# Optimization experiments

Measured on AMD Instinct MI355X. Metric: run time of the kernel, lower is better.

The kernel has to match this reference:

```python
import jax, jax.numpy as jnp
import numpy as np

K_SIZE = 5  # kernel_size


def _patches(f, k):
    # f: (b, c, h, w) -> (b, c, k*k, h, w), matching torch.nn.Unfold ordering
    # (patch positions row-major (kh, kw) per channel), padding = k//2, stride 1.
    p = k // 2
    b, c, h, w = f.shape
    fp = jnp.pad(f, ((0, 0), (0, 0), (p, p), (p, p)))
    slices = [fp[:, :, i:i + h, j:j + w] for i in range(k) for j in range(k)]
    return jnp.stack(slices, axis=2)


def _conv1x1(w, b, f):
    # w: (out, in), b: (out,), f: (b, in, h, w)
    return jnp.einsum('oc,bchw->bohw', w, f) + b[None, :, None, None]


def setup_inputs() -> dict:
    key = jax.random.key(0)
    ks = jax.random.split(key, 8)
    B, XC, YC, FT, H, W = 4, 64, 64, 64, 128, 128
    x = jax.random.normal(ks[0], (B, XC, H, W), dtype=jnp.float32)
    y = jax.random.normal(ks[1], (B, YC, H, W), dtype=jnp.float32)
    sx = 1.0 / np.sqrt(XC)
    sy = 1.0 / np.sqrt(YC)
    sf = 1.0 / np.sqrt(FT)
    wx = jax.random.uniform(ks[2], (FT, XC), jnp.float32, -sx, sx)
    bx = jax.random.uniform(ks[3], (FT,), jnp.float32, -sx, sx)
    wy = jax.random.uniform(ks[4], (FT, YC), jnp.float32, -sy, sy)
    by = jax.random.uniform(ks[5], (FT,), jnp.float32, -sy, sy)
    wo = jax.random.uniform(ks[6], (XC, FT), jnp.float32, -sf, sf)
    bo = jax.random.uniform(ks[7], (XC,), jnp.float32, -sf, sf)
    return {"x": x, "y": y, "wx": wx, "bx": bx, "wy": wy, "by": by, "wo": wo, "bo": bo}


def reference(x, y, wx, bx, wy, by, wo, bo):
    k = K_SIZE
    q = _conv1x1(wy, by, y)            # (b, feat, h, w): Q (the q axis of size 1 is squeezed)
    Kp = _patches(q, k)                # (b, feat, k^2, h, w): unfold(conv_y(y))
    v = _conv1x1(wx, bx, x)            # (b, feat, h, w)
    Vp = _patches(v, k)                # (b, feat, k^2, h, w): unfold(conv_x(x))
    A = jnp.einsum('bckhw,bchw->bkhw', Kp, q)   # scores over k^2 neighbors
    A = jax.nn.softmax(A, axis=1)               # softmax over dim=1 (k^2)
    out = jnp.einsum('bkhw,bckhw->bchw', A, Vp)  # aggregate values
    out = _conv1x1(wo, bo, out)
    return out + x
```

## Files before the change

kernel.cpp:

```cpp
#include <hip/hip_runtime.h>

#define HH   128
#define WW   128
#define HW   (HH * WW)
#define CC   64
#define TILE 8
#define HALO 12
#define NHP  (HALO * HALO)

typedef unsigned int uint32;
typedef _Float16 h2   __attribute__((ext_vector_type(2)));
typedef __fp16   h2b  __attribute__((ext_vector_type(2)));
typedef _Float16 h8   __attribute__((ext_vector_type(8)));
typedef float    f32x4 __attribute__((ext_vector_type(4)));

__device__ __forceinline__ uint32 pkrtz(float a, float b) {
    h2b r = __builtin_amdgcn_cvt_pkrtz(a, b);
    return __builtin_bit_cast(uint32, r);
}
__device__ __forceinline__ float dot2(uint32 a, uint32 b, float c) {
#if __has_builtin(__builtin_amdgcn_fdot2)
    return __builtin_amdgcn_fdot2(__builtin_bit_cast(h2b, a),
                                  __builtin_bit_cast(h2b, b), c, false);
#else
    h2 x = __builtin_bit_cast(h2, a), y = __builtin_bit_cast(h2, b);
    return c + (float)x.x * (float)y.x + (float)x.y * (float)y.y;
#endif
}
__device__ __forceinline__ f32x4 mfma16(uint4 a, uint4 b, f32x4 c) {
    return __builtin_amdgcn_mfma_f32_16x16x32_f16(
        __builtin_bit_cast(h8, a), __builtin_bit_cast(h8, b), c, 0, 0, 0);
}
__device__ __forceinline__ uint4 pack_w8(const float* __restrict__ w) {
    const float4 lo = *(const float4*)w;
    const float4 hi = *(const float4*)(w + 4);
    uint4 r;
    r.x = pkrtz(lo.x, lo.y); r.y = pkrtz(lo.z, lo.w);
    r.z = pkrtz(hi.x, hi.y); r.w = pkrtz(hi.z, hi.w);
    return r;
}

__global__ __launch_bounds__(256, 4)
void fused_attn(const float* __restrict__ x, const float* __restrict__ y,
                const float* __restrict__ wx, const float* __restrict__ bx,
                const float* __restrict__ wy, const float* __restrict__ by,
                const float* __restrict__ wo, const float* __restrict__ bo,
                float* __restrict__ out)
{
    __shared__ uint32 Ah[NHP * 32];
    __shared__ uint32 Bh[NHP * 32];

    const int lin  = blockIdx.x;
    const int xcd  = lin & 7;
    const int rr   = lin >> 3;
    const int b    = xcd >> 1;
    const int half = xcd & 1;
    const int ty0  = (((rr >> 4) + half * 8)) * TILE;
    const int tx0  = (rr & 15) * TILE;

    const int t = threadIdx.x;

    for (int i = t; i < NHP * 8; i += 256) {
        const int c   = i / NHP;
        const int pix = i - c * NHP;
        const int hy  = pix / HALO, hx = pix - hy * HALO;
        int gy = ty0 + hy - 2, gx = tx0 + hx - 2;
        const bool ok = ((unsigned)gy < HH) & ((unsigned)gx < WW);
        if (!ok) { gy = 0; gx = 0; }
        const size_t base = (size_t)b * CC * HW + (size_t)(c * 8) * HW
                          + (size_t)gy * WW + gx;
        float yv[8], xv[8];
        #pragma unroll
        for (int j = 0; j < 8; ++j) {
            yv[j] = y[base + (size_t)j * HW];
            xv[j] = x[base + (size_t)j * HW];
        }
        uint4 yq, xq;
        yq.x = pkrtz(yv[0], yv[1]); yq.y = pkrtz(yv[2], yv[3]);
        yq.z = pkrtz(yv[4], yv[5]); yq.w = pkrtz(yv[6], yv[7]);
        xq.x = pkrtz(xv[0], xv[1]); xq.y = pkrtz(xv[2], xv[3]);
        xq.z = pkrtz(xv[4], xv[5]); xq.w = pkrtz(xv[6], xv[7]);
        const int w0 = (c ^ (pix & 7)) * 4;
        *(uint4*)&Ah[pix * 32 + w0] = yq;
        *(uint4*)&Bh[pix * 32 + w0] = xq;
    }
    __syncthreads();

    const int wv = t >> 6;
    const int ln = t & 63;
    const int lm = ln & 15;
    const int qd = ln >> 4;

    f32x4 accq[9], accv[9];
    uint2 xres[4];
    {
        const uint4 aq0 = pack_w8(wy + (wv * 16 + lm) * CC + qd * 8);
        const uint4 aq1 = pack_w8(wy + (wv * 16 + lm) * CC + qd * 8 + 32);
        const uint4 av0 = pack_w8(wx + (wv * 16 + lm) * CC + qd * 8);
        const uint4 av1 = pack_w8(wx + (wv * 16 + lm) * CC + qd * 8 + 32);
        #pragma unroll
        for (int nt = 0; nt < 9; ++nt) {
            const int px = nt * 16 + lm, sw = px & 7;
            const uint4 b0 = *(const uint4*)&Ah[px * 32 + ((qd    ) ^ sw) * 4];
            const uint4 b1 = *(const uint4*)&Ah[px * 32 + ((qd + 4) ^ sw) * 4];
            f32x4 a = {0.f, 0.f, 0.f, 0.f};
            a = mfma16(aq0, b0, a); a = mfma16(aq1, b1, a); accq[nt] = a;
            const uint4 c0 = *(const uint4*)&Bh[px * 32 + ((qd    ) ^ sw) * 4];
            const uint4 c1 = *(const uint4*)&Bh[px * 32 + ((qd + 4) ^ sw) * 4];
            f32x4 v = {0.f, 0.f, 0.f, 0.f};
            v = mfma16(av0, c0, v); v = mfma16(av1, c1, v); accv[nt] = v;
        }
        #pragma unroll
        for (int nt = 0; nt < 4; ++nt) {
            const int px = nt * 16 + lm;
            const int hpix = ((px >> 3) + 2) * HALO + (px & 7) + 2;
            const int chunk = wv * 2 + (qd >> 1);
            xres[nt] = *(const uint2*)
                &Bh[hpix * 32 + (chunk ^ (hpix & 7)) * 4 + (qd & 1) * 2];
        }
    }
    __syncthreads();

    {
        const float4 bq = *(const float4*)(by + wv * 16 + qd * 4);
        const float4 bv = *(const float4*)(bx + wv * 16 + qd * 4);
        const int chunk = wv * 2 + (qd >> 1);
        #pragma unroll
        for (int nt = 0; nt < 9; ++nt) {
            const int px = nt * 16 + lm;
            const int hy = px / HALO, hx = px - hy * HALO;
            const int gy = ty0 + hy - 2, gx = tx0 + hx - 2;
            uint2 wq = {0u, 0u}, wvv = {0u, 0u};
            if (((unsigned)gy < HH) & ((unsigned)gx < WW)) {
                wq.x  = pkrtz(accq[nt].x + bq.x, accq[nt].y + bq.y);
                wq.y  = pkrtz(accq[nt].z + bq.z, accq[nt].w + bq.w);
                wvv.x = pkrtz(accv[nt].x + bv.x, accv[nt].y + bv.y);
                wvv.y = pkrtz(accv[nt].z + bv.z, accv[nt].w + bv.w);
            }
            const int off = px * 32 + (chunk ^ (px & 7)) * 4 + (qd & 1) * 2;
            *(uint2*)&Ah[off] = wq;
            *(uint2*)&Bh[off] = wvv;
        }
    }
    __syncthreads();

    const int p    = t >> 2, sub = t & 3;
    const int py   = p >> 3, px8 = p & 7;
    const int crow = (py + 2) * HALO + (px8 + 2);

    uint32 qc[8];
    {
        const int c0 = ((2 * sub) ^ (crow & 7)) * 4;
        const int c1 = ((2 * sub + 1) ^ (crow & 7)) * 4;
        *(uint4*)&qc[0] = *(const uint4*)&Ah[crow * 32 + c0];
        *(uint4*)&qc[4] = *(const uint4*)&Ah[crow * 32 + c1];
    }

    float sc[25];
    #pragma unroll
    for (int dy = 0; dy < 5; ++dy)
        #pragma unroll
        for (int dx = 0; dx < 5; ++dx) {
            const int nrow = (py + dy) * HALO + (px8 + dx);
            const int c0 = ((2 * sub) ^ (nrow & 7)) * 4;
            const int c1 = ((2 * sub + 1) ^ (nrow & 7)) * 4;
            const uint4 r0 = *(const uint4*)&Ah[nrow * 32 + c0];
            const uint4 r1 = *(const uint4*)&Ah[nrow * 32 + c1];
            float s = 0.f;
            s = dot2(qc[0], r0.x, s); s = dot2(qc[1], r0.y, s);
            s = dot2(qc[2], r0.z, s); s = dot2(qc[3], r0.w, s);
            s = dot2(qc[4], r1.x, s); s = dot2(qc[5], r1.y, s);
            s = dot2(qc[6], r1.z, s); s = dot2(qc[7], r1.w, s);
            s += __shfl_xor(s, 1);
            s += __shfl_xor(s, 2);
            sc[dy * 5 + dx] = s;
        }

    float mx = sc[0];
    #pragma unroll
    for (int k = 1; k < 25; ++k) mx = fmaxf(mx, sc[k]);
    float sum = 0.f;
    #pragma unroll
    for (int k = 0; k < 25; ++k) { sc[k] = __expf(sc[k] - mx); sum += sc[k]; }
    const float inv = 1.f / sum;

    h2 ag[8];
    #pragma unroll
    for (int k = 0; k < 8; ++k) ag[k] = (h2)(_Float16)0;
    #pragma unroll
    for (int dy = 0; dy < 5; ++dy)
        #pragma unroll
        for (int dx = 0; dx < 5; ++dx) {
            const int nrow = (py + dy) * HALO + (px8 + dx);
            const int c0 = ((2 * sub) ^ (nrow & 7)) * 4;
            const int c1 = ((2 * sub + 1) ^ (nrow & 7)) * 4;
            const uint4 r0 = *(const uint4*)&Bh[nrow * 32 + c0];
            const uint4 r1 = *(const uint4*)&Bh[nrow * 32 + c1];
            const _Float16 af = (_Float16)(sc[dy * 5 + dx] * inv);
            const h2 a2 = {af, af};
            ag[0] += a2 * __builtin_bit_cast(h2, r0.x);
            ag[1] += a2 * __builtin_bit_cast(h2, r0.y);
            ag[2] += a2 * __builtin_bit_cast(h2, r0.z);
            ag[3] += a2 * __builtin_bit_cast(h2, r0.w);
            ag[4] += a2 * __builtin_bit_cast(h2, r1.x);
            ag[5] += a2 * __builtin_bit_cast(h2, r1.y);
            ag[6] += a2 * __builtin_bit_cast(h2, r1.z);
            ag[7] += a2 * __builtin_bit_cast(h2, r1.w);
        }

    __syncthreads();
    {
        const int c0 = ((2 * sub) ^ (p & 7)) * 4;
        const int c1 = ((2 * sub + 1) ^ (p & 7)) * 4;
        uint4 w0, w1;
        w0.x = __builtin_bit_cast(uint32, ag[0]); w0.y = __builtin_bit_cast(uint32, ag[1]);
        w0.z = __builtin_bit_cast(uint32, ag[2]); w0.w = __builtin_bit_cast(uint32, ag[3]);
        w1.x = __builtin_bit_cast(uint32, ag[4]); w1.y = __builtin_bit_cast(uint32, ag[5]);
        w1.z = __builtin_bit_cast(uint32, ag[6]); w1.w = __builtin_bit_cast(uint32, ag[7]);
        *(uint4*)&Ah[p * 32 + c0] = w0;
        *(uint4*)&Ah[p * 32 + c1] = w1;
    }
    __syncthreads();

    {
        const uint4 a0 = pack_w8(wo + (wv * 16 + lm) * CC + qd * 8);
        const uint4 a1 = pack_w8(wo + (wv * 16 + lm) * CC + qd * 8 + 32);
        const float4 bq = *(const float4*)(bo + wv * 16 + qd * 4);
        #pragma unroll
        for (int nt = 0; nt < 4; ++nt) {
            const int px = nt * 16 + lm, sw = px & 7;
            const uint4 b0 = *(const uint4*)&Ah[px * 32 + ((qd    ) ^ sw) * 4];
            const uint4 b1 = *(const uint4*)&Ah[px * 32 + ((qd + 4) ^ sw) * 4];
            f32x4 a = {0.f, 0.f, 0.f, 0.f};
            a = mfma16(a0, b0, a);
            a = mfma16(a1, b1, a);
            const int gh = ty0 + (px >> 3), gw = tx0 + (px & 7);
            const h2 xp0 = __builtin_bit_cast(h2, xres[nt].x);
            const h2 xp1 = __builtin_bit_cast(h2, xres[nt].y);
            const float rv[4] = {(float)xp0.x, (float)xp0.y,
                                 (float)xp1.x, (float)xp1.y};
            const float av4[4] = {a.x + bq.x, a.y + bq.y, a.z + bq.z, a.w + bq.w};
            #pragma unroll
            for (int r = 0; r < 4; ++r) {
                const int oc = wv * 16 + qd * 4 + r;
                const size_t ad = (size_t)(b * CC + oc) * HW + (size_t)gh * WW + gw;
                out[ad] = av4[r] + rv[r];
            }
        }
    }
}

extern "C" void kernel_launch(void* const* d_in, const int* in_sizes, int n_in,
                              void* d_out, int out_size, void* d_ws, size_t ws_size,
                              hipStream_t stream) {
    const float* x  = (const float*)d_in[0];
    const float* y  = (const float*)d_in[1];
    const float* wx = (const float*)d_in[2];
    const float* bx = (const float*)d_in[3];
    const float* wy = (const float*)d_in[4];
    const float* by = (const float*)d_in[5];
    const float* wo = (const float*)d_in[6];
    const float* bo = (const float*)d_in[7];
    float* out = (float*)d_out;
    (void)d_ws; (void)ws_size;

    fused_attn<<<dim3(1024), 256, 0, stream>>>(x, y, wx, bx, wy, by, wo, bo, out);
}
```

Measured before the change: 115.9 us.

## Split Q and V projections into separate phases to overlap V with scoring

Separates the Q and V 1x1-conv MFMA phases so that Q is finished and written to shared memory first. The V projection then runs before a barrier placed after the softmax, which lets the score and softmax work interleave with V writes across waves and cuts the live accumulator registers from 18 to 9 vectors. The softmax normalization moves from each of the 25 weights to a single half-precision multiply on the 8 aggregated values. This adds an extra barrier and changes fp16 rounding, since unnormalized exponentials are accumulated in fp16 before scaling.

```diff
diff --git a/kernel.cpp b/kernel.cpp
--- a/kernel.cpp
+++ b/kernel.cpp
@@ -90,14 +90,12 @@
     const int ln = t & 63;
     const int lm = ln & 15;
     const int qd = ln >> 4;
-
-    f32x4 accq[9], accv[9];
-    uint2 xres[4];
+    const int chunk = wv * 2 + (qd >> 1);
+
     {
         const uint4 aq0 = pack_w8(wy + (wv * 16 + lm) * CC + qd * 8);
         const uint4 aq1 = pack_w8(wy + (wv * 16 + lm) * CC + qd * 8 + 32);
-        const uint4 av0 = pack_w8(wx + (wv * 16 + lm) * CC + qd * 8);
-        const uint4 av1 = pack_w8(wx + (wv * 16 + lm) * CC + qd * 8 + 32);
+        f32x4 accq[9];
         #pragma unroll
         for (int nt = 0; nt < 9; ++nt) {
             const int px = nt * 16 + lm, sw = px & 7;
@@ -105,6 +103,31 @@
             const uint4 b1 = *(const uint4*)&Ah[px * 32 + ((qd + 4) ^ sw) * 4];
             f32x4 a = {0.f, 0.f, 0.f, 0.f};
             a = mfma16(aq0, b0, a); a = mfma16(aq1, b1, a); accq[nt] = a;
+        }
+        __syncthreads();
+        const float4 bq = *(const float4*)(by + wv * 16 + qd * 4);
+        #pragma unroll
+        for (int nt = 0; nt < 9; ++nt) {
+            const int px = nt * 16 + lm;
+            const int hy = px / HALO, hx = px - hy * HALO;
+            const int gy = ty0 + hy - 2, gx = tx0 + hx - 2;
+            uint2 wq = {0u, 0u};
+            if (((unsigned)gy < HH) & ((unsigned)gx < WW)) {
+                wq.x = pkrtz(accq[nt].x + bq.x, accq[nt].y + bq.y);
+                wq.y = pkrtz(accq[nt].z + bq.z, accq[nt].w + bq.w);
+            }
+            *(uint2*)&Ah[px * 32 + (chunk ^ (px & 7)) * 4 + (qd & 1) * 2] = wq;
+        }
+    }
+
+    uint2 xres[4];
+    {
+        const uint4 av0 = pack_w8(wx + (wv * 16 + lm) * CC + qd * 8);
+        const uint4 av1 = pack_w8(wx + (wv * 16 + lm) * CC + qd * 8 + 32);
+        f32x4 accv[9];
+        #pragma unroll
+        for (int nt = 0; nt < 9; ++nt) {
+            const int px = nt * 16 + lm, sw = px & 7;
             const uint4 c0 = *(const uint4*)&Bh[px * 32 + ((qd    ) ^ sw) * 4];
             const uint4 c1 = *(const uint4*)&Bh[px * 32 + ((qd + 4) ^ sw) * 4];
             f32x4 v = {0.f, 0.f, 0.f, 0.f};
@@ -114,35 +137,24 @@
         for (int nt = 0; nt < 4; ++nt) {
             const int px = nt * 16 + lm;
             const int hpix = ((px >> 3) + 2) * HALO + (px & 7) + 2;
-            const int chunk = wv * 2 + (qd >> 1);
             xres[nt] = *(const uint2*)
                 &Bh[hpix * 32 + (chunk ^ (hpix & 7)) * 4 + (qd & 1) * 2];
         }
-    }
-    __syncthreads();
-
-    {
-        const float4 bq = *(const float4*)(by + wv * 16 + qd * 4);
+        __syncthreads();
         const float4 bv = *(const float4*)(bx + wv * 16 + qd * 4);
-        const int chunk = wv * 2 + (qd >> 1);
         #pragma unroll
         for (int nt = 0; nt < 9; ++nt) {
             const int px = nt * 16 + lm;
             const int hy = px / HALO, hx = px - hy * HALO;
             const int gy = ty0 + hy - 2, gx = tx0 + hx - 2;
-            uint2 wq = {0u, 0u}, wvv = {0u, 0u};
+            uint2 wvv = {0u, 0u};
             if (((unsigned)gy < HH) & ((unsigned)gx < WW)) {
-                wq.x  = pkrtz(accq[nt].x + bq.x, accq[nt].y + bq.y);
-                wq.y  = pkrtz(accq[nt].z + bq.z, accq[nt].w + bq.w);
                 wvv.x = pkrtz(accv[nt].x + bv.x, accv[nt].y + bv.y);
                 wvv.y = pkrtz(accv[nt].z + bv.z, accv[nt].w + bv.w);
             }
-            const int off = px * 32 + (chunk ^ (px & 7)) * 4 + (qd & 1) * 2;
-            *(uint2*)&Ah[off] = wq;
-            *(uint2*)&Bh[off] = wvv;
-        }
-    }
-    __syncthreads();
+            *(uint2*)&Bh[px * 32 + (chunk ^ (px & 7)) * 4 + (qd & 1) * 2] = wvv;
+        }
+    }
 
     const int p    = t >> 2, sub = t & 3;
     const int py   = p >> 3, px8 = p & 7;
@@ -184,6 +196,8 @@
     for (int k = 0; k < 25; ++k) { sc[k] = __expf(sc[k] - mx); sum += sc[k]; }
     const float inv = 1.f / sum;
 
+    __syncthreads();
+
     h2 ag[8];
     #pragma unroll
     for (int k = 0; k < 8; ++k) ag[k] = (h2)(_Float16)0;
@@ -196,7 +210,7 @@
             const int c1 = ((2 * sub + 1) ^ (nrow & 7)) * 4;
             const uint4 r0 = *(const uint4*)&Bh[nrow * 32 + c0];
             const uint4 r1 = *(const uint4*)&Bh[nrow * 32 + c1];
-            const _Float16 af = (_Float16)(sc[dy * 5 + dx] * inv);
+            const _Float16 af = (_Float16)sc[dy * 5 + dx];
             const h2 a2 = {af, af};
             ag[0] += a2 * __builtin_bit_cast(h2, r0.x);
             ag[1] += a2 * __builtin_bit_cast(h2, r0.y);
@@ -210,6 +224,10 @@
 
     __syncthreads();
     {
+        const _Float16 ih = (_Float16)inv;
+        const h2 i2 = {ih, ih};
+        #pragma unroll
+        for (int k = 0; k < 8; ++k) ag[k] *= i2;
         const int c0 = ((2 * sub) ^ (p & 7)) * 4;
         const int c1 = ((2 * sub + 1) ^ (p & 7)) * 4;
         uint4 w0, w1;
```

After: 119.5 us. +3.1%, slower.

## Transpose output MFMA for float4 stores, hoist weight loads, defer softmax normalization

Applied to the files above, without the earlier changes.

Swaps the MFMA operands in the output projection so that each lane holds four consecutive pixels of one output channel. This lets the result be written with a single float4 store instead of four scattered scalar stores, and the residual x values are gathered from LDS to match that layout. It also hoists all weight and bias loads to the kernel start so they overlap the halo load. The 1/sum softmax scale moves from each of the 25 neighbor weights to a single multiply of the fp16 accumulators, which changes rounding slightly.

```diff
diff --git a/kernel.cpp b/kernel.cpp
--- a/kernel.cpp
+++ b/kernel.cpp
@@ -58,7 +58,22 @@
     const int ty0  = (((rr >> 4) + half * 8)) * TILE;
     const int tx0  = (rr & 15) * TILE;
 
-    const int t = threadIdx.x;
+    const int t  = threadIdx.x;
+    const int wv = t >> 6;
+    const int ln = t & 63;
+    const int lm = ln & 15;
+    const int qd = ln >> 4;
+    const int chunk = wv * 2 + (qd >> 1);
+
+    const uint4 aq0 = pack_w8(wy + (wv * 16 + lm) * CC + qd * 8);
+    const uint4 aq1 = pack_w8(wy + (wv * 16 + lm) * CC + qd * 8 + 32);
+    const uint4 av0 = pack_w8(wx + (wv * 16 + lm) * CC + qd * 8);
+    const uint4 av1 = pack_w8(wx + (wv * 16 + lm) * CC + qd * 8 + 32);
+    const uint4 ao0 = pack_w8(wo + (wv * 16 + lm) * CC + qd * 8);
+    const uint4 ao1 = pack_w8(wo + (wv * 16 + lm) * CC + qd * 8 + 32);
+    const float4 bq = *(const float4*)(by + wv * 16 + qd * 4);
+    const float4 bv = *(const float4*)(bx + wv * 16 + qd * 4);
+    const float  boL = bo[wv * 16 + lm];
 
     for (int i = t; i < NHP * 8; i += 256) {
         const int c   = i / NHP;
@@ -86,18 +101,9 @@
     }
     __syncthreads();
 
-    const int wv = t >> 6;
-    const int ln = t & 63;
-    const int lm = ln & 15;
-    const int qd = ln >> 4;
-
     f32x4 accq[9], accv[9];
-    uint2 xres[4];
-    {
-        const uint4 aq0 = pack_w8(wy + (wv * 16 + lm) * CC + qd * 8);
-        const uint4 aq1 = pack_w8(wy + (wv * 16 + lm) * CC + qd * 8 + 32);
-        const uint4 av0 = pack_w8(wx + (wv * 16 + lm) * CC + qd * 8);
-        const uint4 av1 = pack_w8(wx + (wv * 16 + lm) * CC + qd * 8 + 32);
+    float xres[16];
+    {
         #pragma unroll
         for (int nt = 0; nt < 9; ++nt) {
             const int px = nt * 16 + lm, sw = px & 7;
@@ -110,21 +116,22 @@
             f32x4 v = {0.f, 0.f, 0.f, 0.f};
             v = mfma16(av0, c0, v); v = mfma16(av1, c1, v); accv[nt] = v;
         }
-        #pragma unroll
-        for (int nt = 0; nt < 4; ++nt) {
-            const int px = nt * 16 + lm;
-            const int hpix = ((px >> 3) + 2) * HALO + (px & 7) + 2;
-            const int chunk = wv * 2 + (qd >> 1);
-            xres[nt] = *(const uint2*)
-                &Bh[hpix * 32 + (chunk ^ (hpix & 7)) * 4 + (qd & 1) * 2];
-        }
-    }
-    __syncthreads();
-
-    {
-        const float4 bq = *(const float4*)(by + wv * 16 + qd * 4);
-        const float4 bv = *(const float4*)(bx + wv * 16 + qd * 4);
-        const int chunk = wv * 2 + (qd >> 1);
+        const int c8  = wv * 2 + (lm >> 3);
+        const int wrd = (lm & 7) >> 1;
+        #pragma unroll
+        for (int nt = 0; nt < 4; ++nt)
+            #pragma unroll
+            for (int r = 0; r < 4; ++r) {
+                const int p2   = nt * 16 + qd * 4 + r;
+                const int hpix = ((p2 >> 3) + 2) * HALO + (p2 & 7) + 2;
+                const uint32 w = Bh[hpix * 32 + ((c8 ^ (hpix & 7)) << 2) + wrd];
+                const h2 pr = __builtin_bit_cast(h2, w);
+                xres[nt * 4 + r] = (lm & 1) ? (float)pr.y : (float)pr.x;
+            }
+    }
+    __syncthreads();
+
+    {
         #pragma unroll
         for (int nt = 0; nt < 9; ++nt) {
             const int px = nt * 16 + lm;
@@ -196,7 +203,7 @@
             const int c1 = ((2 * sub + 1) ^ (nrow & 7)) * 4;
             const uint4 r0 = *(const uint4*)&Bh[nrow * 32 + c0];
             const uint4 r1 = *(const uint4*)&Bh[nrow * 32 + c1];
-            const _Float16 af = (_Float16)(sc[dy * 5 + dx] * inv);
+            const _Float16 af = (_Float16)sc[dy * 5 + dx];
             const h2 a2 = {af, af};
             ag[0] += a2 * __builtin_bit_cast(h2, r0.x);
             ag[1] += a2 * __builtin_bit_cast(h2, r0.y);
@@ -210,6 +217,10 @@
 
     __syncthreads();
     {
+        const _Float16 ih = (_Float16)inv;
+        const h2 i2 = {ih, ih};
+        #pragma unroll
+        for (int k = 0; k < 8; ++k) ag[k] *= i2;
         const int c0 = ((2 * sub) ^ (p & 7)) * 4;
         const int c1 = ((2 * sub + 1) ^ (p & 7)) * 4;
         uint4 w0, w1;
@@ -223,29 +234,23 @@
     __syncthreads();
 
     {
-        const uint4 a0 = pack_w8(wo + (wv * 16 + lm) * CC + qd * 8);
-        const uint4 a1 = pack_w8(wo + (wv * 16 + lm) * CC + qd * 8 + 32);
-        const float4 bq = *(const float4*)(bo + wv * 16 + qd * 4);
+        const int oc = wv * 16 + lm;
         #pragma unroll
         for (int nt = 0; nt < 4; ++nt) {
             const int px = nt * 16 + lm, sw = px & 7;
             const uint4 b0 = *(const uint4*)&Ah[px * 32 + ((qd    ) ^ sw) * 4];
             const uint4 b1 = *(const uint4*)&Ah[px * 32 + ((qd + 4) ^ sw) * 4];
             f32x4 a = {0.f, 0.f, 0.f, 0.f};
-            a = mfma16(a0, b0, a);
-            a = mfma16(a1, b1, a);
-            const int gh = ty0 + (px >> 3), gw = tx0 + (px & 7);
-            const h2 xp0 = __builtin_bit_cast(h2, xres[nt].x);
-            const h2 xp1 = __builtin_bit_cast(h2, xres[nt].y);
-            const float rv[4] = {(float)xp0.x, (float)xp0.y,
-                                 (float)xp1.x, (float)xp1.y};
-            const float av4[4] = {a.x + bq.x, a.y + bq.y, a.z + bq.z, a.w + bq.w};
-            #pragma unroll
-            for (int r = 0; r < 4; ++r) {
-                const int oc = wv * 16 + qd * 4 + r;
-                const size_t ad = (size_t)(b * CC + oc) * HW + (size_t)gh * WW + gw;
-                out[ad] = av4[r] + rv[r];
-            }
+            a = mfma16(b0, ao0, a);
+            a = mfma16(b1, ao1, a);
+            const int gh  = ty0 + nt * 2 + (qd >> 1);
+            const int gw0 = tx0 + (qd & 1) * 4;
+            float4 o4;
+            o4.x = a.x + boL + xres[nt * 4 + 0];
+            o4.y = a.y + boL + xres[nt * 4 + 1];
+            o4.z = a.z + boL + xres[nt * 4 + 2];
+            o4.w = a.w + boL + xres[nt * 4 + 3];
+            *(float4*)&out[(size_t)(b * CC + oc) * HW + (size_t)gh * WW + gw0] = o4;
         }
     }
 }
```

Result: slower. 124.6 us (+7.6%).
